# Kernel tuning notes

Measured on AMD Instinct MI355X. Metric: run time of the kernel, lower is better.

## Reference

```python
import jax, jax.numpy as jnp
import numpy as np

ALPHA = 0.25
GAMMA = 1.5


def box_iou(a, b):
    # a: [A,4], b: [G,4] in xyxy; torchvision-style IoU
    area_a = (a[:, 2] - a[:, 0]) * (a[:, 3] - a[:, 1])  # [A]
    area_b = (b[:, 2] - b[:, 0]) * (b[:, 3] - b[:, 1])  # [G]
    lt = jnp.maximum(a[:, None, :2], b[None, :, :2])    # [A,G,2]
    rb = jnp.minimum(a[:, None, 2:], b[None, :, 2:])    # [A,G,2]
    wh = jnp.clip(rb - lt, 0.0)
    inter = wh[..., 0] * wh[..., 1]                      # [A,G]
    return inter / (area_a[:, None] + area_b[None, :] - inter)


def setup_inputs() -> dict:
    key = jax.random.key(0)
    ks = jax.random.split(key, 7)
    B, A, C, G = 8, 120000, 80, 32
    classifications = jax.random.uniform(ks[0], (B, A, C), minval=1e-4, maxval=1.0 - 1e-4, dtype=jnp.float32)
    regressions = jax.random.normal(ks[1], (B, A, 4), dtype=jnp.float32)
    actr = jax.random.uniform(ks[2], (A, 2), minval=0.0, maxval=512.0)
    awh = jax.random.uniform(ks[3], (A, 2), minval=16.0, maxval=128.0)
    anchors = jnp.concatenate([actr - 0.5 * awh, actr + 0.5 * awh], axis=-1)[None]  # [1,A,4]
    bctr = jax.random.uniform(ks[4], (B, G, 2), minval=0.0, maxval=512.0)
    bwh = jax.random.uniform(ks[5], (B, G, 2), minval=8.0, maxval=256.0)
    boxes = jnp.concatenate([bctr - 0.5 * bwh, bctr + 0.5 * bwh], axis=-1)  # [B,G,4]
    labels = jax.random.randint(ks[6], (B, G), 0, C, dtype=jnp.int32)
    return {"classifications": classifications, "regressions": regressions,
            "anchors": anchors, "boxes": boxes, "labels": labels}


def focal_loss(classifications, regressions, anchors, boxes, labels):
    anchor = anchors[0]                         # [A,4]
    num_classes = classifications.shape[-1]
    aw = anchor[:, 2] - anchor[:, 0]
    ah = anchor[:, 3] - anchor[:, 1]
    acx = anchor[:, 0] + 0.5 * aw
    acy = anchor[:, 1] + 0.5 * ah

    def per_sample(cls, reg, bx, lb):
        iou = box_iou(anchor, bx)               # [A,G]
        iou_max = jnp.max(iou, axis=1)
        iou_argmax = jnp.argmax(iou, axis=1)
        pos = iou_max >= 0.5                    # [A]
        num_pos = jnp.sum(pos.astype(cls.dtype))

        assigned = bx[iou_argmax]               # [A,4] gather
        onehot = jax.nn.one_hot(lb[iou_argmax], num_classes, dtype=cls.dtype)
        base = jnp.where(iou_max < 0.4, 0.0, -1.0)[:, None]  # ignore by default
        targets = jnp.where(pos[:, None], onehot, base)      # [A,C]

        alpha_factor = jnp.where(targets == 1.0, ALPHA, 1.0 - ALPHA)
        focal_weight = jnp.where(targets == 1.0, 1.0 - cls, cls)
        focal_weight = alpha_factor * focal_weight ** GAMMA
        bce = -(targets * jnp.log(jnp.clip(cls, 1e-6, 1.0))
                + (1.0 - targets) * jnp.log(jnp.clip(1.0 - cls, 1e-6, 1.0)))
        cls_loss = jnp.where(targets != -1.0, focal_weight * bce, 0.0)
        cls_loss = jnp.sum(cls_loss) / jnp.maximum(num_pos, 1.0)

        gw_raw = assigned[:, 2] - assigned[:, 0]
        gh_raw = assigned[:, 3] - assigned[:, 1]
        gcx = assigned[:, 0] + 0.5 * gw_raw
        gcy = assigned[:, 1] + 0.5 * gh_raw
        gw = jnp.clip(gw_raw, 1.0)
        gh = jnp.clip(gh_raw, 1.0)
        tdx = (gcx - acx) / aw
        tdy = (gcy - acy) / ah
        tdw = jnp.log(gw / aw)
        tdh = jnp.log(gh / ah)
        tgt = jnp.stack([tdx, tdy, tdw, tdh], axis=1)   # [A,4]
        diff = jnp.abs(tgt - reg)
        rl = jnp.where(diff <= 1.0 / 9.0, 0.5 * 9.0 * diff ** 2, diff - 0.5 / 9.0)
        # mean over positive anchors' 4 coords (0 if no positives)
        reg_loss = jnp.sum(rl * pos[:, None].astype(rl.dtype)) / (4.0 * jnp.maximum(num_pos, 1.0))
        return cls_loss, reg_loss

    cls_l, reg_l = jax.vmap(per_sample)(classifications, regressions, boxes, labels)
    return jnp.mean(cls_l, axis=0, keepdims=True), jnp.mean(reg_l, axis=0, keepdims=True)


def reference(classifications, regressions, anchors, boxes, labels):
    return focal_loss(classifications, regressions, anchors, boxes, labels)
```

## Files before the change

### kernel.cpp

```cpp
#include <hip/hip_runtime.h>
#include <math.h>

#define B_N 8
#define A_N 120000
#define C_N 80
#define G_N 32


__device__ __forceinline__ float smoothl1(float d) {
    return (d <= (1.0f / 9.0f)) ? 4.5f * d * d : d - (0.5f / 9.0f);
}

__device__ __forceinline__ float focal_term(float p, bool ispos) {
    float q  = 1.0f - p;
    float t  = ispos ? q : p;
    float lg = ispos ? p : q;
    float al = ispos ? 0.25f : 0.75f;
    return al * t * sqrtf(t) * (-__logf(fmaxf(lg, 1e-6f)));
}

__global__ void init_kernel(float* __restrict__ acc) {
    if (threadIdx.x < 24) acc[threadIdx.x] = 0.0f;
}

__global__ __launch_bounds__(256) void fused_kernel(
        const float* __restrict__ anchors,
        const float* __restrict__ regressions,
        const float* __restrict__ cls,
        const float* __restrict__ boxes,
        const int*   __restrict__ labels,
        float*       __restrict__ acc) {
    __shared__ float4      sbox[G_N];
    __shared__ int         slab[G_N];
    __shared__ float       sarea[G_N];
    __shared__ signed char sstate[256];
    __shared__ float2      sred2[4];
    __shared__ float       sred[4];

    const int b      = blockIdx.y;
    const int tid    = threadIdx.x;
    const int base_a = blockIdx.x << 8;

    if (tid < G_N) {
        float4 bx = ((const float4*)boxes)[b * G_N + tid];
        sbox[tid]  = bx;
        slab[tid]  = labels[b * G_N + tid];
        sarea[tid] = (bx.z - bx.x) * (bx.w - bx.y);
    }
    __syncthreads();

    const int a = base_a + tid;
    float my_reg = 0.0f;
    float my_pos = 0.0f;
    signed char st = -1;

    if (a < A_N) {
        float4 an = ((const float4*)anchors)[a];
        float area_a = (an.z - an.x) * (an.w - an.y);
        float best = -1.0f;
        int bestg = 0;
        #pragma unroll 8
        for (int g = 0; g < G_N; ++g) {
            float4 bx = sbox[g];
            float ltx = fmaxf(an.x, bx.x);
            float lty = fmaxf(an.y, bx.y);
            float rbx = fminf(an.z, bx.z);
            float rby = fminf(an.w, bx.w);
            float w = fmaxf(rbx - ltx, 0.0f);
            float h = fmaxf(rby - lty, 0.0f);
            float inter = w * h;
            float iou = inter / (area_a + sarea[g] - inter);
            if (iou > best) { best = iou; bestg = g; }
        }

        if (best >= 0.5f) {
            st = (signed char)slab[bestg];
            my_pos = 1.0f;
            float4 bx = sbox[bestg];
            float aw  = an.z - an.x;
            float ah  = an.w - an.y;
            float acx = an.x + 0.5f * aw;
            float acy = an.y + 0.5f * ah;
            float gwr = bx.z - bx.x;
            float ghr = bx.w - bx.y;
            float gcx = bx.x + 0.5f * gwr;
            float gcy = bx.y + 0.5f * ghr;
            float gw  = fmaxf(gwr, 1.0f);
            float gh  = fmaxf(ghr, 1.0f);
            float t0 = (gcx - acx) / aw;
            float t1 = (gcy - acy) / ah;
            float t2 = __logf(gw / aw);
            float t3 = __logf(gh / ah);
            float4 rg = ((const float4*)regressions)[(size_t)b * A_N + a];
            my_reg = smoothl1(fabsf(t0 - rg.x)) + smoothl1(fabsf(t1 - rg.y))
                   + smoothl1(fabsf(t2 - rg.z)) + smoothl1(fabsf(t3 - rg.w));
        } else {
            st = (best < 0.4f) ? (signed char)(-2) : (signed char)(-1);
        }
    }
    sstate[tid] = st;

    #pragma unroll
    for (int off = 32; off > 0; off >>= 1) {
        my_reg += __shfl_down(my_reg, off);
        my_pos += __shfl_down(my_pos, off);
    }
    if ((tid & 63) == 0) sred2[tid >> 6] = make_float2(my_reg, my_pos);
    __syncthreads();
    if (tid == 0) {
        float r = sred2[0].x + sred2[1].x + sred2[2].x + sred2[3].x;
        float p = sred2[0].y + sred2[1].y + sred2[2].y + sred2[3].y;
        atomicAdd(&acc[8 + b],  r);
        atomicAdd(&acc[16 + b], p);
    }

    const int n_anch = min(256, A_N - base_a);
    const int n4 = n_anch * 20;
    const float4* p4 = (const float4*)(cls + (size_t)b * A_N * C_N) + (size_t)base_a * 20;

    float sum = 0.0f;
    for (int i = tid; i < n4; i += 256) {
        int al    = i / 20;
        int cbase = (i - al * 20) * 4;
        int s = sstate[al];
        if (s == -1) continue;
        float4 v = p4[i];
        sum += focal_term(v.x, s == cbase);
        sum += focal_term(v.y, s == cbase + 1);
        sum += focal_term(v.z, s == cbase + 2);
        sum += focal_term(v.w, s == cbase + 3);
    }

    #pragma unroll
    for (int off = 32; off > 0; off >>= 1) sum += __shfl_down(sum, off);
    if ((tid & 63) == 0) sred[tid >> 6] = sum;
    __syncthreads();
    if (tid == 0) {
        atomicAdd(&acc[b], sred[0] + sred[1] + sred[2] + sred[3]);
    }
}

__global__ void finalize_kernel(const float* __restrict__ acc,
                                float*       __restrict__ out) {
    if (threadIdx.x == 0 && blockIdx.x == 0) {
        float cl = 0.0f, rl = 0.0f;
        #pragma unroll
        for (int b = 0; b < B_N; ++b) {
            float np = fmaxf(acc[16 + b], 1.0f);
            cl += acc[b] / np;
            rl += acc[8 + b] / (4.0f * np);
        }
        out[0] = cl * (1.0f / B_N);
        out[1] = rl * (1.0f / B_N);
    }
}

extern "C" void kernel_launch(void* const* d_in, const int* in_sizes, int n_in,
                              void* d_out, int out_size, void* d_ws, size_t ws_size,
                              hipStream_t stream) {
    const float* cls = (const float*)d_in[0];
    const float* reg = (const float*)d_in[1];
    const float* anc = (const float*)d_in[2];
    const float* box = (const float*)d_in[3];
    const int*   lab = (const int*)d_in[4];
    float* out = (float*)d_out;

    float* acc = (float*)d_ws;

    hipLaunchKernelGGL(init_kernel, dim3(1), dim3(32), 0, stream, acc);

    dim3 g((A_N + 255) / 256, B_N);
    hipLaunchKernelGGL(fused_kernel, g, dim3(256), 0, stream,
                       anc, reg, cls, box, lab, acc);

    hipLaunchKernelGGL(finalize_kernel, dim3(1), dim3(64), 0, stream, acc, out);
}
```

Baseline: 461.3 us.

## Replace atomics with per-block partials, use nontemporal branchless class loads

Each block now writes its partial focal, regression and positive-count sums to its own workspace slot. A parallel finalize kernel reduces those slots, which removes the init kernel and the global atomics. The classification loop drops the skip branch for ignored anchors, loading every element with a nontemporal load and masking by multiplication, and is unrolled by 4. This trades extra memory traffic and math on ignored anchors for a branch-free, better-pipelined streaming loop.

```diff
diff --git a/kernel.cpp b/kernel.cpp
--- a/kernel.cpp
+++ b/kernel.cpp
@@ -5,6 +5,10 @@
 #define A_N 120000
 #define C_N 80
 #define G_N 32
+#define NBX 469
+#define NB  (NBX * B_N)
+
+typedef float f4_t __attribute__((ext_vector_type(4)));
 
 
 __device__ __forceinline__ float smoothl1(float d) {
@@ -19,17 +23,13 @@
     return al * t * sqrtf(t) * (-__logf(fmaxf(lg, 1e-6f)));
 }
 
-__global__ void init_kernel(float* __restrict__ acc) {
-    if (threadIdx.x < 24) acc[threadIdx.x] = 0.0f;
-}
-
 __global__ __launch_bounds__(256) void fused_kernel(
         const float* __restrict__ anchors,
         const float* __restrict__ regressions,
         const float* __restrict__ cls,
         const float* __restrict__ boxes,
         const int*   __restrict__ labels,
-        float*       __restrict__ acc) {
+        float*       __restrict__ ws) {
     __shared__ float4      sbox[G_N];
     __shared__ int         slab[G_N];
     __shared__ float       sarea[G_N];
@@ -40,6 +40,7 @@
     const int b      = blockIdx.y;
     const int tid    = threadIdx.x;
     const int base_a = blockIdx.x << 8;
+    const int blk    = b * NBX + blockIdx.x;
 
     if (tid < G_N) {
         float4 bx = ((const float4*)boxes)[b * G_N + tid];
@@ -108,27 +109,26 @@
     if ((tid & 63) == 0) sred2[tid >> 6] = make_float2(my_reg, my_pos);
     __syncthreads();
     if (tid == 0) {
-        float r = sred2[0].x + sred2[1].x + sred2[2].x + sred2[3].x;
-        float p = sred2[0].y + sred2[1].y + sred2[2].y + sred2[3].y;
-        atomicAdd(&acc[8 + b],  r);
-        atomicAdd(&acc[16 + b], p);
+        ws[NB + blk]     = sred2[0].x + sred2[1].x + sred2[2].x + sred2[3].x;
+        ws[2 * NB + blk] = sred2[0].y + sred2[1].y + sred2[2].y + sred2[3].y;
     }
 
     const int n_anch = min(256, A_N - base_a);
     const int n4 = n_anch * 20;
-    const float4* p4 = (const float4*)(cls + (size_t)b * A_N * C_N) + (size_t)base_a * 20;
+    const f4_t* p4 = (const f4_t*)(cls + (size_t)b * A_N * C_N) + (size_t)base_a * 20;
 
     float sum = 0.0f;
+    #pragma unroll 4
     for (int i = tid; i < n4; i += 256) {
         int al    = i / 20;
         int cbase = (i - al * 20) * 4;
         int s = sstate[al];
-        if (s == -1) continue;
-        float4 v = p4[i];
-        sum += focal_term(v.x, s == cbase);
-        sum += focal_term(v.y, s == cbase + 1);
-        sum += focal_term(v.z, s == cbase + 2);
-        sum += focal_term(v.w, s == cbase + 3);
+        f4_t v = __builtin_nontemporal_load(&p4[i]);
+        float m = (s == -1) ? 0.0f : 1.0f;
+        sum += m * (focal_term(v.x, s == cbase)
+                  + focal_term(v.y, s == cbase + 1)
+                  + focal_term(v.z, s == cbase + 2)
+                  + focal_term(v.w, s == cbase + 3));
     }
 
     #pragma unroll
@@ -136,20 +136,42 @@
     if ((tid & 63) == 0) sred[tid >> 6] = sum;
     __syncthreads();
     if (tid == 0) {
-        atomicAdd(&acc[b], sred[0] + sred[1] + sred[2] + sred[3]);
+        ws[blk] = sred[0] + sred[1] + sred[2] + sred[3];
     }
 }
 
-__global__ void finalize_kernel(const float* __restrict__ acc,
-                                float*       __restrict__ out) {
-    if (threadIdx.x == 0 && blockIdx.x == 0) {
-        float cl = 0.0f, rl = 0.0f;
+__global__ __launch_bounds__(256) void finalize_kernel(
+        const float* __restrict__ ws, float* __restrict__ out) {
+    __shared__ float s0[4], s1[4], s2[4];
+    const int tid = threadIdx.x;
+    float cl = 0.0f, rl = 0.0f;
+
+    for (int b = 0; b < B_N; ++b) {
+        float sc = 0.0f, sr = 0.0f, sp = 0.0f;
+        for (int i = tid; i < NBX; i += 256) {
+            sc += ws[b * NBX + i];
+            sr += ws[NB + b * NBX + i];
+            sp += ws[2 * NB + b * NBX + i];
+        }
         #pragma unroll
-        for (int b = 0; b < B_N; ++b) {
-            float np = fmaxf(acc[16 + b], 1.0f);
-            cl += acc[b] / np;
-            rl += acc[8 + b] / (4.0f * np);
+        for (int off = 32; off > 0; off >>= 1) {
+            sc += __shfl_down(sc, off);
+            sr += __shfl_down(sr, off);
+            sp += __shfl_down(sp, off);
         }
+        if ((tid & 63) == 0) { s0[tid >> 6] = sc; s1[tid >> 6] = sr; s2[tid >> 6] = sp; }
+        __syncthreads();
+        if (tid == 0) {
+            float c = s0[0] + s0[1] + s0[2] + s0[3];
+            float r = s1[0] + s1[1] + s1[2] + s1[3];
+            float p = s2[0] + s2[1] + s2[2] + s2[3];
+            float np = fmaxf(p, 1.0f);
+            cl += c / np;
+            rl += r / (4.0f * np);
+        }
+        __syncthreads();
+    }
+    if (tid == 0) {
         out[0] = cl * (1.0f / B_N);
         out[1] = rl * (1.0f / B_N);
     }
@@ -165,13 +187,11 @@
     const int*   lab = (const int*)d_in[4];
     float* out = (float*)d_out;
 
-    float* acc = (float*)d_ws;
+    float* ws = (float*)d_ws;
 
-    hipLaunchKernelGGL(init_kernel, dim3(1), dim3(32), 0, stream, acc);
+    dim3 g(NBX, B_N);
+    hipLaunchKernelGGL(fused_kernel, g, dim3(256), 0, stream,
+                       anc, reg, cls, box, lab, ws);
 
-    dim3 g((A_N + 255) / 256, B_N);
-    hipLaunchKernelGGL(fused_kernel, g, dim3(256), 0, stream,
-                       anc, reg, cls, box, lab, acc);
-
-    hipLaunchKernelGGL(finalize_kernel, dim3(1), dim3(64), 0, stream, acc, out);
+    hipLaunchKernelGGL(finalize_kernel, dim3(1), dim3(256), 0, stream, ws, out);
 }
```

Result: no change. 456.9 us (-0.9%).
